# Kernel optimization log

Hardware: AMD Instinct MI355X
Metric: run time of the kernel (lower is better)

## Reference

```python
import jax, jax.numpy as jnp
import numpy as np

B, N, D_MODEL, HIDDEN = 4, 1024, 1024, 1024
N_HEAD, D_KEY, D_VALUE = 16, 64, 64


def setup_inputs() -> dict:
    key = jax.random.key(0)
    ks = jax.random.split(key, 12)
    s = 0.02
    return {
        "queries": jax.random.normal(ks[0], (B, N, D_MODEL), jnp.float32),
        "keys": jax.random.normal(ks[1], (B, N, HIDDEN), jnp.float32),
        "values": jax.random.normal(ks[2], (B, N, HIDDEN), jnp.float32),
        "attn_bias": jax.random.normal(ks[3], (B, N_HEAD, N, N), jnp.float32),
        "Wq": jax.random.normal(ks[4], (D_MODEL, D_KEY * N_HEAD), jnp.float32) * s,
        "bq": jnp.zeros((D_KEY * N_HEAD,), jnp.float32),
        "Wk": jax.random.normal(ks[5], (HIDDEN, D_KEY * N_HEAD), jnp.float32) * s,
        "bk": jnp.zeros((D_KEY * N_HEAD,), jnp.float32),
        "Wv": jax.random.normal(ks[6], (HIDDEN, D_VALUE * N_HEAD), jnp.float32) * s,
        "bv": jnp.zeros((D_VALUE * N_HEAD,), jnp.float32),
        "Wo": jax.random.normal(ks[7], (max(D_MODEL, HIDDEN), D_MODEL), jnp.float32) * s,
        "bo": jnp.zeros((D_MODEL,), jnp.float32),
    }


def reference(queries, keys, values, attn_bias, Wq, bq, Wk, bk, Wv, bv, Wo, bo):
    b, n, _ = queries.shape
    # QKV projections, split heads -> [b, h, n, d]
    q = (queries @ Wq + bq).reshape(b, n, N_HEAD, D_KEY).transpose(0, 2, 1, 3)
    k = (keys @ Wk + bk).reshape(b, keys.shape[1], N_HEAD, D_KEY).transpose(0, 2, 1, 3)
    v = (values @ Wv + bv).reshape(b, values.shape[1], N_HEAD, D_VALUE).transpose(0, 2, 1, 3)
    # scaled dot-product attention with additive bias (dropout_rate=0 -> identity)
    scaled_q = q * (D_KEY ** -0.5)
    product = jnp.einsum("bhqd,bhkd->bhqk", scaled_q, k) + attn_bias
    weights = jax.nn.softmax(product, axis=-1)
    ctx = jnp.einsum("bhqk,bhkd->bhqd", weights, v)
    # combine heads -> [b, n, h*d]
    out = ctx.transpose(0, 2, 1, 3).reshape(b, n, N_HEAD * D_VALUE)
    return out @ Wo + bo
```

## Files before the change

### kernel.cpp

```cpp
#include <hip/hip_runtime.h>
#include <cstdint>
#include <type_traits>


typedef unsigned short u16;
typedef __attribute__((ext_vector_type(8))) short v8bf;
typedef __attribute__((ext_vector_type(4))) float v4f;

#define DEV static __device__ __forceinline__

DEV u16 f2b(float f) {
    union { float f; uint32_t u; } v; v.f = f;
    uint32_t r = v.u + 0x7FFFu + ((v.u >> 16) & 1u);
    return (u16)(r >> 16);
}

DEV void gl_lds16(const void* g, void* l) {
    __builtin_amdgcn_global_load_lds((const __attribute__((address_space(1))) void*)g,
                                     (__attribute__((address_space(3))) void*)l, 16, 0, 0);
}

__global__ __launch_bounds__(256) void transpose_w4(const float* __restrict__ w0, const float* __restrict__ w1,
                                                    const float* __restrict__ w2, const float* __restrict__ w3,
                                                    u16* __restrict__ o0, u16* __restrict__ o1,
                                                    u16* __restrict__ o2, u16* __restrict__ o3) {
    __shared__ float tile[32][33];
    const float* in = blockIdx.z == 0 ? w0 : blockIdx.z == 1 ? w1 : blockIdx.z == 2 ? w2 : w3;
    u16* out        = blockIdx.z == 0 ? o0 : blockIdx.z == 1 ? o1 : blockIdx.z == 2 ? o2 : o3;
    const int tx = threadIdx.x, ty = threadIdx.y;
    const int n0 = blockIdx.x * 32, k0 = blockIdx.y * 32;
#pragma unroll
    for (int i = 0; i < 4; i++)
        tile[ty + i * 8][tx] = in[(size_t)(k0 + ty + i * 8) * 1024 + n0 + tx];
    __syncthreads();
#pragma unroll
    for (int i = 0; i < 4; i++)
        out[(size_t)(n0 + ty + i * 8) * 1024 + k0 + tx] = f2b(tile[tx][ty + i * 8]);
}

__global__ __launch_bounds__(256) void cast3(const float* __restrict__ a0, const float* __restrict__ a1,
                                             const float* __restrict__ a2,
                                             u16* __restrict__ o0, u16* __restrict__ o1, u16* __restrict__ o2) {
    const int z = blockIdx.y;
    const float* in = z == 0 ? a0 : z == 1 ? a1 : a2;
    u16* out        = z == 0 ? o0 : z == 1 ? o1 : o2;
    const size_t i = ((size_t)blockIdx.x * 256 + threadIdx.x) * 8;
    const float4 f0 = *reinterpret_cast<const float4*>(in + i);
    const float4 f1 = *reinterpret_cast<const float4*>(in + i + 4);
    union { u16 h[8]; uint4 v4; } pk;
    pk.h[0] = f2b(f0.x); pk.h[1] = f2b(f0.y); pk.h[2] = f2b(f0.z); pk.h[3] = f2b(f0.w);
    pk.h[4] = f2b(f1.x); pk.h[5] = f2b(f1.y); pk.h[6] = f2b(f1.z); pk.h[7] = f2b(f1.w);
    *reinterpret_cast<uint4*>(out + i) = pk.v4;
}

template <int BN, typename TO>
DEV void gemm_body(const u16* __restrict__ A, const u16* __restrict__ Bt,
                   const float* __restrict__ bias, TO* __restrict__ C,
                   u16* __restrict__ Ct, float cscale, bool storeT,
                   u16* aS, u16* bS) {
    constexpr int FJ = BN / 32;
    const int tid = threadIdx.x;
    const int wave = tid >> 6, lane = tid & 63, l16 = lane & 15, quad = lane >> 4;
    const int m0 = blockIdx.x * 128, n0 = blockIdx.y * BN;
    const int wr = wave >> 1, wc = wave & 1;
    const int r8 = lane >> 3, c8 = lane & 7;

    v4f acc[4][FJ];
#pragma unroll
    for (int i = 0; i < 4; i++)
#pragma unroll
        for (int j = 0; j < FJ; j++) acc[i][j] = (v4f){0.f, 0.f, 0.f, 0.f};

    for (int kk = 0; kk < 1024; kk += 64) {
        if (kk) __syncthreads();
#pragma unroll
        for (int cl = 0; cl < 4; cl++) {
            const int row = wave * 32 + cl * 8 + r8;
            gl_lds16(A + (size_t)(m0 + row) * 1024 + kk + ((c8 ^ (row & 7)) * 8),
                     aS + (wave * 32 + cl * 8) * 64);
        }
#pragma unroll
        for (int cl = 0; cl < BN / 32; cl++) {
            const int row = wave * (BN / 4) + cl * 8 + r8;
            gl_lds16(Bt + (size_t)(n0 + row) * 1024 + kk + ((c8 ^ (row & 7)) * 8),
                     bS + (wave * (BN / 4) + cl * 8) * 64);
        }
        __syncthreads();
#pragma unroll
        for (int kt = 0; kt < 2; kt++) {
            v8bf af[4], bf[FJ];
#pragma unroll
            for (int i = 0; i < 4; i++) {
                const int row = wr * 64 + i * 16 + l16;
                af[i] = *reinterpret_cast<const v8bf*>(aS + row * 64 + (((kt * 4 + quad) ^ (row & 7)) * 8));
            }
#pragma unroll
            for (int j = 0; j < FJ; j++) {
                const int row = wc * (BN / 2) + j * 16 + l16;
                bf[j] = *reinterpret_cast<const v8bf*>(bS + row * 64 + (((kt * 4 + quad) ^ (row & 7)) * 8));
            }
#pragma unroll
            for (int i = 0; i < 4; i++)
#pragma unroll
                for (int j = 0; j < FJ; j++)
                    acc[i][j] = __builtin_amdgcn_mfma_f32_16x16x32_bf16(af[i], bf[j], acc[i][j], 0, 0, 0);
        }
    }
    float bv[FJ];
#pragma unroll
    for (int j = 0; j < FJ; j++) bv[j] = bias[n0 + wc * (BN / 2) + j * 16 + l16];
    if (storeT) {
#pragma unroll
        for (int i = 0; i < 4; i++)
#pragma unroll
            for (int j = 0; j < FJ; j++) {
                const int col = n0 + wc * (BN / 2) + j * 16 + l16;
                const int row0 = m0 + wr * 64 + i * 16 + quad * 4;
                union { u16 h[4]; uint2 u; } pk;
#pragma unroll
                for (int r = 0; r < 4; r++) pk.h[r] = f2b((acc[i][j][r] + bv[j]) * cscale);
                *reinterpret_cast<uint2*>(&Ct[(size_t)col * 4096 + row0]) = pk.u;
            }
    } else {
#pragma unroll
        for (int i = 0; i < 4; i++)
#pragma unroll
            for (int j = 0; j < FJ; j++) {
                const int col = n0 + wc * (BN / 2) + j * 16 + l16;
#pragma unroll
                for (int r = 0; r < 4; r++) {
                    const int row = m0 + wr * 64 + i * 16 + quad * 4 + r;
                    const float val = (acc[i][j][r] + bv[j]) * cscale;
                    if constexpr (std::is_same_v<TO, u16>) C[(size_t)row * 1024 + col] = f2b(val);
                    else                                   C[(size_t)row * 1024 + col] = val;
                }
            }
    }
}

__global__ __launch_bounds__(256, 3) void gemm_qkv(
    const u16* __restrict__ Qc, const u16* __restrict__ Kc, const u16* __restrict__ Vc,
    const u16* __restrict__ WqT, const u16* __restrict__ WkT, const u16* __restrict__ WvT,
    const float* __restrict__ bq, const float* __restrict__ bk, const float* __restrict__ bv,
    u16* __restrict__ Qb, u16* __restrict__ Kb, u16* __restrict__ VT) {
    __shared__ __align__(16) u16 aS[128 * 64];
    __shared__ __align__(16) u16 bS[128 * 64];
    const int z = blockIdx.z;
    const u16* A    = z == 0 ? Qc : z == 1 ? Kc : Vc;
    const u16* Bt   = z == 0 ? WqT : z == 1 ? WkT : WvT;
    const float* bi = z == 0 ? bq : z == 1 ? bk : bv;
    u16* Cn         = z == 0 ? Qb : Kb;
    gemm_body<128, u16>(A, Bt, bi, Cn, VT, z == 0 ? 0.125f : 1.0f, z == 2, aS, bS);
}

__global__ __launch_bounds__(256, 3) void gemm_out(const u16* __restrict__ A, const u16* __restrict__ Bt,
                                                   const float* __restrict__ bias, float* __restrict__ C) {
    __shared__ __align__(16) u16 aS[128 * 64];
    __shared__ __align__(16) u16 bS[64 * 64];
    gemm_body<64, float>(A, Bt, bias, C, nullptr, 1.0f, false, aS, bS);
}

__global__ __launch_bounds__(256, 2) void attn2(const u16* __restrict__ Q,
                                                const u16* __restrict__ K,
                                                const u16* __restrict__ VT,
                                                const float* __restrict__ bias,
                                                u16* __restrict__ ctx) {
    __shared__ __align__(16) u16 kS[2][64 * 64];
    __shared__ __align__(16) u16 vS[2][64 * 64];
    __shared__ __align__(16) float biasS[2][64 * 64];
    __shared__ __align__(16) u16 pT[4][16 * 72];

    const int tid = threadIdx.x;
    const int wave = tid >> 6, lane = tid & 63, l16 = lane & 15, quad = lane >> 4;
    const int bh = blockIdx.x, q0 = blockIdx.y * 64;
    const int b = bh >> 4, h = bh & 15;
    const int r8 = lane >> 3, c8 = lane & 7;
    const int r16 = lane >> 4, c16 = lane & 15;

    v8bf qf[2];
    {
        const size_t qrow = ((size_t)(b * 1024 + q0 + wave * 16 + l16)) * 1024 + h * 64;
        qf[0] = *reinterpret_cast<const v8bf*>(Q + qrow + quad * 8);
        qf[1] = *reinterpret_cast<const v8bf*>(Q + qrow + 32 + quad * 8);
    }

    v4f ctxacc[4];
#pragma unroll
    for (int v = 0; v < 4; v++) ctxacc[v] = (v4f){0.f, 0.f, 0.f, 0.f};
    float rs = 0.f;

    const size_t kg = ((size_t)b * 1024) * 1024 + h * 64;
    const size_t vg = ((size_t)h * 64) * 4096 + b * 1024;
    const float* bp = bias + ((size_t)bh * 1024 + q0) * 1024;
    u16* pw = pT[wave];

    auto stage = [&](int c, int buf) {
        const int nc = c * 64;
#pragma unroll
        for (int cl = 0; cl < 2; cl++) {
            const int key = wave * 16 + cl * 8 + r8;
            gl_lds16(K + kg + (size_t)(nc + key) * 1024 + ((c8 ^ (key & 7)) * 8),
                     kS[buf] + (wave * 16 + cl * 8) * 64);
        }
#pragma unroll
        for (int cl = 0; cl < 2; cl++) {
            const int d = wave * 16 + cl * 8 + r8;
            gl_lds16(VT + vg + (size_t)d * 4096 + nc + ((c8 ^ (d & 7)) * 8),
                     vS[buf] + (wave * 16 + cl * 8) * 64);
        }
#pragma unroll
        for (int cl = 0; cl < 4; cl++) {
            const int row = wave * 16 + cl * 4 + r16;
            gl_lds16(bp + (size_t)row * 1024 + nc + ((c16 ^ (row & 15)) * 4),
                     biasS[buf] + (wave * 16 + cl * 4) * 64);
        }
    };

    stage(0, 0);
    asm volatile("s_waitcnt vmcnt(0)" ::: "memory");
    __builtin_amdgcn_s_barrier();

    for (int c = 0; c < 16; c++) {
        const int buf = c & 1;
        if (c < 15) stage(c + 1, buf ^ 1);

#pragma unroll
        for (int t = 0; t < 4; t++) {
            v4f s = (v4f){0.f, 0.f, 0.f, 0.f};
            __builtin_amdgcn_s_setprio(1);
#pragma unroll
            for (int kt = 0; kt < 2; kt++) {
                const int krow = t * 16 + l16;
                const v8bf kf = *reinterpret_cast<const v8bf*>(
                    kS[buf] + krow * 64 + (((kt * 4 + quad) ^ (krow & 7)) * 8));
                s = __builtin_amdgcn_mfma_f32_16x16x32_bf16(kf, qf[kt], s, 0, 0, 0);
            }
            __builtin_amdgcn_s_setprio(0);
            const float4 bi = *reinterpret_cast<const float4*>(
                biasS[buf] + (wave * 16 + l16) * 64 + (((t * 4 + quad) ^ l16) * 4));
            const float p0 = __expf(s[0] + bi.x);
            const float p1 = __expf(s[1] + bi.y);
            const float p2 = __expf(s[2] + bi.z);
            const float p3 = __expf(s[3] + bi.w);
            rs += (p0 + p1) + (p2 + p3);
            union { u16 h[4]; uint2 u; } pk;
            pk.h[0] = f2b(p0); pk.h[1] = f2b(p1); pk.h[2] = f2b(p2); pk.h[3] = f2b(p3);
            *reinterpret_cast<uint2*>(pw + l16 * 72 + t * 16 + quad * 4) = pk.u;
        }
#pragma unroll
        for (int kt = 0; kt < 2; kt++) {
            const v8bf pf = *reinterpret_cast<const v8bf*>(pw + l16 * 72 + kt * 32 + quad * 8);
            __builtin_amdgcn_s_setprio(1);
#pragma unroll
            for (int v = 0; v < 4; v++) {
                const int drow = v * 16 + l16;
                const v8bf vf = *reinterpret_cast<const v8bf*>(
                    vS[buf] + drow * 64 + (((kt * 4 + quad) ^ (drow & 7)) * 8));
                ctxacc[v] = __builtin_amdgcn_mfma_f32_16x16x32_bf16(pf, vf, ctxacc[v], 0, 0, 0);
            }
            __builtin_amdgcn_s_setprio(0);
        }
        if (c < 15) {
            asm volatile("s_waitcnt vmcnt(0)" ::: "memory");
            __builtin_amdgcn_s_barrier();
        }
    }

    rs += __shfl_xor(rs, 16);
    rs += __shfl_xor(rs, 32);
    float dninv[4];
#pragma unroll
    for (int r = 0; r < 4; r++) dninv[r] = 1.f / __shfl(rs, quad * 4 + r, 16);
#pragma unroll
    for (int v = 0; v < 4; v++)
#pragma unroll
        for (int r = 0; r < 4; r++) {
            const int row = q0 + wave * 16 + quad * 4 + r;
            ctx[((size_t)(b * 1024 + row)) * 1024 + h * 64 + v * 16 + l16] =
                f2b(ctxacc[v][r] * dninv[r]);
        }
}

extern "C" void kernel_launch(void* const* d_in, const int* in_sizes, int n_in,
                              void* d_out, int out_size, void* d_ws, size_t ws_size,
                              hipStream_t stream) {
    const float* queries = (const float*)d_in[0];
    const float* keys    = (const float*)d_in[1];
    const float* values  = (const float*)d_in[2];
    const float* abias   = (const float*)d_in[3];
    const float* Wq = (const float*)d_in[4];
    const float* bq = (const float*)d_in[5];
    const float* Wk = (const float*)d_in[6];
    const float* bk = (const float*)d_in[7];
    const float* Wv = (const float*)d_in[8];
    const float* bv = (const float*)d_in[9];
    const float* Wo = (const float*)d_in[10];
    const float* bo = (const float*)d_in[11];
    float* out = (float*)d_out;

    char* ws = (char*)d_ws;
    u16* Qb   = (u16*)(ws);
    u16* Kb   = (u16*)(ws + (size_t)(8u << 20));
    u16* VTb  = (u16*)(ws + (size_t)(16u << 20));
    u16* ctxb = (u16*)(ws + (size_t)(24u << 20));
    u16* Qc   = (u16*)(ws + (size_t)(32u << 20));
    u16* Kc   = (u16*)(ws + (size_t)(40u << 20));
    u16* Vc   = (u16*)(ws + (size_t)(48u << 20));
    u16* WqT  = (u16*)(ws + (size_t)(56u << 20));
    u16* WkT  = (u16*)(ws + (size_t)(58u << 20));
    u16* WvT  = (u16*)(ws + (size_t)(60u << 20));
    u16* WoT  = (u16*)(ws + (size_t)(62u << 20));

    transpose_w4<<<dim3(32, 32, 4), dim3(32, 8), 0, stream>>>(Wq, Wk, Wv, Wo, WqT, WkT, WvT, WoT);
    cast3<<<dim3(2048, 3), 256, 0, stream>>>(queries, keys, values, Qc, Kc, Vc);
    gemm_qkv<<<dim3(32, 8, 3), 256, 0, stream>>>(Qc, Kc, Vc, WqT, WkT, WvT, bq, bk, bv, Qb, Kb, VTb);
    attn2<<<dim3(64, 16), 256, 0, stream>>>(Qb, Kb, VTb, abias, ctxb);
    gemm_out<<<dim3(32, 16), 256, 0, stream>>>(ctxb, WoT, bo, out);
}
```

Baseline: 493.6 us.

## Load attention bias directly into registers and merge prep kernels

```diff
diff --git a/kernel.cpp b/kernel.cpp
--- a/kernel.cpp
+++ b/kernel.cpp
@@ -20,37 +20,38 @@
                                      (__attribute__((address_space(3))) void*)l, 16, 0, 0);
 }
 
-__global__ __launch_bounds__(256) void transpose_w4(const float* __restrict__ w0, const float* __restrict__ w1,
-                                                    const float* __restrict__ w2, const float* __restrict__ w3,
-                                                    u16* __restrict__ o0, u16* __restrict__ o1,
-                                                    u16* __restrict__ o2, u16* __restrict__ o3) {
+__global__ __launch_bounds__(256) void prep(
+    const float* __restrict__ w0, const float* __restrict__ w1,
+    const float* __restrict__ w2, const float* __restrict__ w3,
+    const float* __restrict__ a0, const float* __restrict__ a1, const float* __restrict__ a2,
+    u16* __restrict__ t0, u16* __restrict__ t1, u16* __restrict__ t2, u16* __restrict__ t3,
+    u16* __restrict__ c0, u16* __restrict__ c1, u16* __restrict__ c2) {
     __shared__ float tile[32][33];
-    const float* in = blockIdx.z == 0 ? w0 : blockIdx.z == 1 ? w1 : blockIdx.z == 2 ? w2 : w3;
-    u16* out        = blockIdx.z == 0 ? o0 : blockIdx.z == 1 ? o1 : blockIdx.z == 2 ? o2 : o3;
-    const int tx = threadIdx.x, ty = threadIdx.y;
-    const int n0 = blockIdx.x * 32, k0 = blockIdx.y * 32;
-#pragma unroll
-    for (int i = 0; i < 4; i++)
-        tile[ty + i * 8][tx] = in[(size_t)(k0 + ty + i * 8) * 1024 + n0 + tx];
-    __syncthreads();
-#pragma unroll
-    for (int i = 0; i < 4; i++)
-        out[(size_t)(n0 + ty + i * 8) * 1024 + k0 + tx] = f2b(tile[tx][ty + i * 8]);
-}
-
-__global__ __launch_bounds__(256) void cast3(const float* __restrict__ a0, const float* __restrict__ a1,
-                                             const float* __restrict__ a2,
-                                             u16* __restrict__ o0, u16* __restrict__ o1, u16* __restrict__ o2) {
-    const int z = blockIdx.y;
-    const float* in = z == 0 ? a0 : z == 1 ? a1 : a2;
-    u16* out        = z == 0 ? o0 : z == 1 ? o1 : o2;
-    const size_t i = ((size_t)blockIdx.x * 256 + threadIdx.x) * 8;
-    const float4 f0 = *reinterpret_cast<const float4*>(in + i);
-    const float4 f1 = *reinterpret_cast<const float4*>(in + i + 4);
-    union { u16 h[8]; uint4 v4; } pk;
-    pk.h[0] = f2b(f0.x); pk.h[1] = f2b(f0.y); pk.h[2] = f2b(f0.z); pk.h[3] = f2b(f0.w);
-    pk.h[4] = f2b(f1.x); pk.h[5] = f2b(f1.y); pk.h[6] = f2b(f1.z); pk.h[7] = f2b(f1.w);
-    *reinterpret_cast<uint4*>(out + i) = pk.v4;
+    const int z = blockIdx.z, tid = threadIdx.x;
+    if (z < 4) {
+        if (blockIdx.x >= 1024) return;
+        const float* in = z == 0 ? w0 : z == 1 ? w1 : z == 2 ? w2 : w3;
+        u16* out        = z == 0 ? t0 : z == 1 ? t1 : z == 2 ? t2 : t3;
+        const int tx = tid & 31, ty = tid >> 5;
+        const int n0 = (blockIdx.x & 31) * 32, k0 = (blockIdx.x >> 5) * 32;
+#pragma unroll
+        for (int i = 0; i < 4; i++)
+            tile[ty + i * 8][tx] = in[(size_t)(k0 + ty + i * 8) * 1024 + n0 + tx];
+        __syncthreads();
+#pragma unroll
+        for (int i = 0; i < 4; i++)
+            out[(size_t)(n0 + ty + i * 8) * 1024 + k0 + tx] = f2b(tile[tx][ty + i * 8]);
+    } else {
+        const float* in = z == 4 ? a0 : z == 5 ? a1 : a2;
+        u16* out        = z == 4 ? c0 : z == 5 ? c1 : c2;
+        const size_t i = ((size_t)blockIdx.x * 256 + tid) * 8;
+        const float4 f0 = *reinterpret_cast<const float4*>(in + i);
+        const float4 f1 = *reinterpret_cast<const float4*>(in + i + 4);
+        union { u16 h[8]; uint4 v4; } pk;
+        pk.h[0] = f2b(f0.x); pk.h[1] = f2b(f0.y); pk.h[2] = f2b(f0.z); pk.h[3] = f2b(f0.w);
+        pk.h[4] = f2b(f1.x); pk.h[5] = f2b(f1.y); pk.h[6] = f2b(f1.z); pk.h[7] = f2b(f1.w);
+        *reinterpret_cast<uint4*>(out + i) = pk.v4;
+    }
 }
 
 template <int BN, typename TO>
@@ -160,14 +161,13 @@
     gemm_body<64, float>(A, Bt, bias, C, nullptr, 1.0f, false, aS, bS);
 }
 
-__global__ __launch_bounds__(256, 2) void attn2(const u16* __restrict__ Q,
+__global__ __launch_bounds__(256, 3) void attn2(const u16* __restrict__ Q,
                                                 const u16* __restrict__ K,
                                                 const u16* __restrict__ VT,
                                                 const float* __restrict__ bias,
                                                 u16* __restrict__ ctx) {
     __shared__ __align__(16) u16 kS[2][64 * 64];
     __shared__ __align__(16) u16 vS[2][64 * 64];
-    __shared__ __align__(16) float biasS[2][64 * 64];
     __shared__ __align__(16) u16 pT[4][16 * 72];
 
     const int tid = threadIdx.x;
@@ -175,7 +175,6 @@
     const int bh = blockIdx.x, q0 = blockIdx.y * 64;
     const int b = bh >> 4, h = bh & 15;
     const int r8 = lane >> 3, c8 = lane & 7;
-    const int r16 = lane >> 4, c16 = lane & 15;
 
     v8bf qf[2];
     {
@@ -191,8 +190,7 @@
 
     const size_t kg = ((size_t)b * 1024) * 1024 + h * 64;
     const size_t vg = ((size_t)h * 64) * 4096 + b * 1024;
-    const float* bp = bias + ((size_t)bh * 1024 + q0) * 1024;
-    u16* pw = pT[wave];
+    const float* bpl = bias + ((size_t)bh * 1024 + q0 + wave * 16 + l16) * 1024 + quad * 4;
 
     auto stage = [&](int c, int buf) {
         const int nc = c * 64;
@@ -208,22 +206,15 @@
             gl_lds16(VT + vg + (size_t)d * 4096 + nc + ((c8 ^ (d & 7)) * 8),
                      vS[buf] + (wave * 16 + cl * 8) * 64);
         }
-#pragma unroll
-        for (int cl = 0; cl < 4; cl++) {
-            const int row = wave * 16 + cl * 4 + r16;
-            gl_lds16(bp + (size_t)row * 1024 + nc + ((c16 ^ (row & 15)) * 4),
-                     biasS[buf] + (wave * 16 + cl * 4) * 64);
-        }
     };
-
-    stage(0, 0);
-    asm volatile("s_waitcnt vmcnt(0)" ::: "memory");
-    __builtin_amdgcn_s_barrier();
-
-    for (int c = 0; c < 16; c++) {
-        const int buf = c & 1;
-        if (c < 15) stage(c + 1, buf ^ 1);
-
+    auto loadBias = [&](int c, float4* br) {
+#pragma unroll
+        for (int t = 0; t < 4; t++)
+            br[t] = *reinterpret_cast<const float4*>(bpl + c * 64 + t * 16);
+    };
+    u16* pw = pT[wave];
+
+    auto compute = [&](const u16* kb, const u16* vb, const float4* br) {
 #pragma unroll
         for (int t = 0; t < 4; t++) {
             v4f s = (v4f){0.f, 0.f, 0.f, 0.f};
@@ -232,12 +223,11 @@
             for (int kt = 0; kt < 2; kt++) {
                 const int krow = t * 16 + l16;
                 const v8bf kf = *reinterpret_cast<const v8bf*>(
-                    kS[buf] + krow * 64 + (((kt * 4 + quad) ^ (krow & 7)) * 8));
+                    kb + krow * 64 + (((kt * 4 + quad) ^ (krow & 7)) * 8));
                 s = __builtin_amdgcn_mfma_f32_16x16x32_bf16(kf, qf[kt], s, 0, 0, 0);
             }
             __builtin_amdgcn_s_setprio(0);
-            const float4 bi = *reinterpret_cast<const float4*>(
-                biasS[buf] + (wave * 16 + l16) * 64 + (((t * 4 + quad) ^ l16) * 4));
+            const float4 bi = br[t];
             const float p0 = __expf(s[0] + bi.x);
             const float p1 = __expf(s[1] + bi.y);
             const float p2 = __expf(s[2] + bi.z);
@@ -255,12 +245,32 @@
             for (int v = 0; v < 4; v++) {
                 const int drow = v * 16 + l16;
                 const v8bf vf = *reinterpret_cast<const v8bf*>(
-                    vS[buf] + drow * 64 + (((kt * 4 + quad) ^ (drow & 7)) * 8));
+                    vb + drow * 64 + (((kt * 4 + quad) ^ (drow & 7)) * 8));
                 ctxacc[v] = __builtin_amdgcn_mfma_f32_16x16x32_bf16(pf, vf, ctxacc[v], 0, 0, 0);
             }
             __builtin_amdgcn_s_setprio(0);
         }
-        if (c < 15) {
+    };
+
+    float4 brA[4], brB[4];
+    stage(0, 0);
+    loadBias(0, brA);
+    asm volatile("s_waitcnt vmcnt(0)" ::: "memory");
+    __builtin_amdgcn_s_barrier();
+
+    for (int cp = 0; cp < 8; cp++) {
+        stage(2 * cp + 1, 1);
+        loadBias(2 * cp + 1, brB);
+        compute(kS[0], vS[0], brA);
+        asm volatile("s_waitcnt vmcnt(0)" ::: "memory");
+        __builtin_amdgcn_s_barrier();
+
+        if (cp < 7) {
+            stage(2 * cp + 2, 0);
+            loadBias(2 * cp + 2, brA);
+        }
+        compute(kS[1], vS[1], brB);
+        if (cp < 7) {
             asm volatile("s_waitcnt vmcnt(0)" ::: "memory");
             __builtin_amdgcn_s_barrier();
         }
@@ -311,8 +321,8 @@
     u16* WvT  = (u16*)(ws + (size_t)(60u << 20));
     u16* WoT  = (u16*)(ws + (size_t)(62u << 20));
 
-    transpose_w4<<<dim3(32, 32, 4), dim3(32, 8), 0, stream>>>(Wq, Wk, Wv, Wo, WqT, WkT, WvT, WoT);
-    cast3<<<dim3(2048, 3), 256, 0, stream>>>(queries, keys, values, Qc, Kc, Vc);
+    prep<<<dim3(2048, 1, 7), 256, 0, stream>>>(Wq, Wk, Wv, Wo, queries, keys, values,
+                                               WqT, WkT, WvT, WoT, Qc, Kc, Vc);
     gemm_qkv<<<dim3(32, 8, 3), 256, 0, stream>>>(Qc, Kc, Vc, WqT, WkT, WvT, bq, bk, bv, Qb, Kb, VTb);
     attn2<<<dim3(64, 16), 256, 0, stream>>>(Qb, Kb, VTb, abias, ctxb);
     gemm_out<<<dim3(32, 16), 256, 0, stream>>>(ctxb, WoT, bo, out);
```

Result: no change. 496.7 us (+0.6%).
